# Optimization experiments

Measured on AMD Instinct MI355X. Metric: run time of the kernel, lower is better.

The kernel has to match this reference:

```python
import jax, jax.numpy as jnp
import numpy as np


def setup_inputs() -> dict:
    key = jax.random.key(0)
    k1, k2 = jax.random.split(key)
    # (t, h, w) per image/video; h, w divisible by spatial_merge_size=2
    grid_thw = jnp.asarray(np.array([[1, 64, 64], [4, 48, 48], [8, 32, 64], [16, 32, 32]], dtype=np.int64))
    num_grid_per_side = 35
    hidden = 1152
    pos_embed_weight = jax.random.normal(k1, (num_grid_per_side * num_grid_per_side, hidden), dtype=jnp.float32)
    quarter_head_dim = 32  # mrope_section [24,20,20] sums to 64 = 2*quarter_head_dim
    inv_freq = 1.0 / (10000.0 ** (jnp.arange(quarter_head_dim, dtype=jnp.float32) / quarter_head_dim))
    return {
        'grid_thw': grid_thw,
        'pos_embed_weight': pos_embed_weight,
        'inv_freq': inv_freq,
        'spatial_merge_size': 2,
        'num_grid_per_side': num_grid_per_side,
    }


def _forward(grid_np, pos_embed_weight, inv_freq, m, G):
    # grid_np: host numpy int array [num_images, 3] -> static per-image shapes
    D = pos_embed_weight.shape[-1]
    pieces = []
    coords_list = []
    for t, h, w in grid_np.tolist():
        # ---- 4-corner bilinear interpolation of pos embeddings ----
        h_idxs = jnp.linspace(0.0, G - 1, h)
        w_idxs = jnp.linspace(0.0, G - 1, w)
        hf = h_idxs.astype(jnp.int32)
        wf = w_idxs.astype(jnp.int32)
        hc = jnp.minimum(hf + 1, G - 1)
        wc = jnp.minimum(wf + 1, G - 1)
        dh = h_idxs - hf.astype(h_idxs.dtype)
        dw = w_idxs - wf.astype(w_idxs.dtype)
        idx = jnp.stack([
            (hf[:, None] * G + wf[None, :]).reshape(-1),
            (hf[:, None] * G + wc[None, :]).reshape(-1),
            (hc[:, None] * G + wf[None, :]).reshape(-1),
            (hc[:, None] * G + wc[None, :]).reshape(-1),
        ], 0)  # [4, h*w]
        wts = jnp.stack([
            ((1 - dh)[:, None] * (1 - dw)[None, :]).reshape(-1),
            ((1 - dh)[:, None] * dw[None, :]).reshape(-1),
            (dh[:, None] * (1 - dw)[None, :]).reshape(-1),
            (dh[:, None] * dw[None, :]).reshape(-1),
        ], 0).astype(pos_embed_weight.dtype)  # [4, h*w]
        pe = (pos_embed_weight[idx] * wts[:, :, None]).sum(0)  # [h*w, D]
        # ---- spatial-merge reshuffle, repeated over t frames ----
        pe = jnp.tile(pe, (t, 1)).reshape(t, h // m, m, w // m, m, D)
        pe = pe.transpose(0, 1, 3, 2, 4, 5).reshape(-1, D)
        pieces.append(pe)
        # ---- (row, col) position ids in merged-block order ----
        br = jnp.arange(h // m)
        bc = jnp.arange(w // m)
        im = jnp.arange(m)
        row = br[:, None, None, None] * m + im[None, None, :, None]
        col = bc[None, :, None, None] * m + im[None, None, None, :]
        row = jnp.broadcast_to(row, (h // m, w // m, m, m)).reshape(-1)
        col = jnp.broadcast_to(col, (h // m, w // m, m, m)).reshape(-1)
        coords = jnp.stack([row, col], -1)  # [h*w, 2]
        coords = jnp.tile(coords, (t, 1))   # [t*h*w, 2]
        coords_list.append(coords)
    patch_pos_embeds = jnp.concatenate(pieces, 0)   # [total_tokens, D]
    pos_ids = jnp.concatenate(coords_list, 0)       # [total_tokens, 2]
    max_hw = int(grid_np[:, 1:].max())
    seq = jnp.arange(max_hw, dtype=jnp.float32)
    freqs = seq[:, None] * inv_freq[None, :]        # [max_hw, Q]
    embeddings = freqs[pos_ids].reshape(pos_ids.shape[0], -1)  # [T, 2Q]
    # MRoPE section interleave: freqs_3d[0..2] are identical copies of
    # `embeddings`, so replacing strided slices of freqs_t with slices of the
    # other copies is a mathematical no-op: freqs_t == embeddings.
    emb = jnp.concatenate([embeddings, embeddings], -1)  # [T, head_dim]
    return patch_pos_embeds, jnp.cos(emb), jnp.sin(emb)


def reference(grid_thw, pos_embed_weight, inv_freq, spatial_merge_size, num_grid_per_side):
    grid_np = np.asarray(grid_thw)  # int grid sizes are static metadata
    return _forward(grid_np, pos_embed_weight, inv_freq, int(spatial_merge_size), int(num_grid_per_side))
```

## Files before the change

kernel.cpp:

```cpp
#include <hip/hip_runtime.h>


typedef float fx4 __attribute__((ext_vector_type(4)));

__device__ __forceinline__ void nt_store4(float* p, fx4 v) {
    __builtin_nontemporal_store(v, (fx4*)p);
}

template <int T, int H, int W, int OFF>
__device__ __forceinline__ void patch_body(int b, const float* __restrict__ tab,
                                           float* __restrict__ out) {
    constexpr int C4 = 1152 / 4;
    constexpr int HW = H * W;
    constexpr int WB = W / 2;

    int idx = b * 256 + (int)threadIdx.x;
    int tok = idx / C4;
    int c4  = idx - tok * C4;

    int j  = tok & 1;
    int i  = (tok >> 1) & 1;
    int blk = tok >> 2;
    int bw = blk % WB;
    int bh = blk / WB;
    int row = (bh << 1) + i;
    int col = (bw << 1) + j;

    float hx = (float)row * (float)(34.0 / (H - 1));
    float wx = (float)col * (float)(34.0 / (W - 1));
    int hf = (int)hx, wf = (int)wx;
    float dh = hx - (float)hf, dw = wx - (float)wf;
    int hc = min(hf + 1, 34), wc = min(wf + 1, 34);

    float w00 = (1.f - dh) * (1.f - dw);
    float w01 = (1.f - dh) * dw;
    float w10 = dh * (1.f - dw);
    float w11 = dh * dw;

    const fx4 a = *((const fx4*)(tab + (hf * 35 + wf) * 1152) + c4);
    const fx4 bq= *((const fx4*)(tab + (hf * 35 + wc) * 1152) + c4);
    const fx4 c = *((const fx4*)(tab + (hc * 35 + wf) * 1152) + c4);
    const fx4 d = *((const fx4*)(tab + (hc * 35 + wc) * 1152) + c4);

    fx4 o = w00 * a + w01 * bq + w10 * c + w11 * d;

    float* dst = out + (size_t)(OFF + tok) * 1152 + (c4 << 2);
    #pragma unroll
    for (int f = 0; f < T; ++f)
        nt_store4(dst + (size_t)f * (HW * 1152), o);
}

template <int T, int H, int W, int OFF>
__device__ __forceinline__ void rope_body(int b, const float* __restrict__ invf,
                                          float* __restrict__ cosO,
                                          float* __restrict__ sinO) {
    constexpr int HW = H * W;
    constexpr int WB = W / 2;

    int idx = b * 256 + (int)threadIdx.x;
    int tok = idx >> 4;
    int l4  = idx & 15;
    int rem = tok % HW;

    int j  = rem & 1;
    int i  = (rem >> 1) & 1;
    int blk = rem >> 2;
    int bw = blk % WB;
    int bh = blk / WB;
    int row = (bh << 1) + i;
    int col = (bw << 1) + j;

    float fp = (float)((l4 < 8) ? row : col);
    fx4 iv = ((const fx4*)invf)[l4 & 7];

    float s0, c0, s1, c1, s2, c2, s3, c3;
    __sincosf(fp * iv.x, &s0, &c0);
    __sincosf(fp * iv.y, &s1, &c1);
    __sincosf(fp * iv.z, &s2, &c2);
    __sincosf(fp * iv.w, &s3, &c3);
    fx4 cv = {c0, c1, c2, c3};
    fx4 sv = {s0, s1, s2, s3};

    size_t base = (size_t)(OFF + tok) * 128 + (l4 << 2);
    nt_store4(cosO + base,      cv);
    nt_store4(cosO + base + 64, cv);
    nt_store4(sinO + base,      sv);
    nt_store4(sinO + base + 64, sv);
}

__global__ __launch_bounds__(256) void fused_kernel(
    const float* __restrict__ tab, const float* __restrict__ invf,
    float* __restrict__ out, float* __restrict__ cosO, float* __restrict__ sinO)
{
    int b = (int)blockIdx.x;
    if      (b < 1152)  patch_body<16,32, 32, 29696>(b,         tab, out);
    else if (b < 3456)  patch_body<8, 32, 64, 13312>(b - 1152,  tab, out);
    else if (b < 6048)  patch_body<4, 48, 48, 4096> (b - 3456,  tab, out);
    else if (b < 7072)  rope_body<16,32, 32, 29696> (b - 6048,  invf, cosO, sinO);
    else if (b < 8096)  rope_body<8, 32, 64, 13312> (b - 7072,  invf, cosO, sinO);
    else if (b < 8672)  rope_body<4, 48, 48, 4096>  (b - 8096,  invf, cosO, sinO);
    else if (b < 8928)  rope_body<1, 64, 64, 0>     (b - 8672,  invf, cosO, sinO);
    else                patch_body<1, 64, 64, 0>    (b - 8928,  tab, out);
}

extern "C" void kernel_launch(void* const* d_in, const int* in_sizes, int n_in,
                              void* d_out, int out_size, void* d_ws, size_t ws_size,
                              hipStream_t stream) {
    const float* tab  = (const float*)d_in[1];
    const float* invf = (const float*)d_in[2];
    float* out = (float*)d_out;

    constexpr size_t NTOK = 46080;
    float* cosO = out + NTOK * 1152;
    float* sinO = cosO + NTOK * 128;

    fused_kernel<<<13536, 256, 0, stream>>>(tab, invf, out, cosO, sinO);
}
```

Baseline: 55.96 us.

## Share bilinear corner loads across 2x2 merge-block tokens in pos-embed interpolation

For images whose side is larger than the grid (step < 1), each thread now computes two or four adjacent tokens of a 2x2 merge block. It loads a 3x3 or 2x3 neighbourhood of table rows and reuses them through separable interpolation, where before every token loaded its own four corners. This cuts gather loads per output and roughly halves the block count. In exchange each thread does more work and holds more registers.

```diff
diff --git a/kernel.cpp b/kernel.cpp
--- a/kernel.cpp
+++ b/kernel.cpp
@@ -8,15 +8,132 @@
 }
 
 template <int T, int H, int W, int OFF>
-__device__ __forceinline__ void patch_body(int b, const float* __restrict__ tab,
-                                           float* __restrict__ out) {
-    constexpr int C4 = 1152 / 4;
-    constexpr int HW = H * W;
-    constexpr int WB = W / 2;
-
-    int idx = b * 256 + (int)threadIdx.x;
-    int tok = idx / C4;
-    int c4  = idx - tok * C4;
+__device__ __forceinline__ void pe_quad_body(int b, const float* __restrict__ tab,
+                                             float* __restrict__ out) {
+    static_assert(H > 35 && W > 35, "2x2 sharing needs step < 1 in both axes");
+    constexpr int HW = H * W;
+    constexpr int WB = W / 2;
+
+    int idx = b * 256 + (int)threadIdx.x;
+    int mb  = idx / 288;
+    int c4  = idx - mb * 288;
+    int bw  = mb % WB;
+    int bh  = mb / WB;
+
+    int row0 = bh << 1, col0 = bw << 1;
+
+    float hx0 = (float)row0 * (float)(34.0 / (H - 1));
+    float hx1 = (float)(row0 + 1) * (float)(34.0 / (H - 1));
+    float wx0 = (float)col0 * (float)(34.0 / (W - 1));
+    float wx1 = (float)(col0 + 1) * (float)(34.0 / (W - 1));
+
+    int hf0 = (int)hx0;  float dh0 = hx0 - (float)hf0;
+    int hf1 = (int)hx1;  float dh1 = hx1 - (float)hf1;
+    int oi  = hf1 - hf0;
+    int wf0 = (int)wx0;  float dw0 = wx0 - (float)wf0;
+    int wf1 = (int)wx1;  float dw1 = wx1 - (float)wf1;
+    int oj  = wf1 - wf0;
+
+    int r1 = min(hf0 + 1, 34), r2 = min(hf0 + 2, 34);
+    int c1 = min(wf0 + 1, 34), c2 = min(wf0 + 2, 34);
+
+    const float* base = tab + c4 * 4;
+    #define LD(r, c) (*((const fx4*)(base + (size_t)((r) * 35 + (c)) * 1152)))
+    fx4 P00 = LD(hf0, wf0), P01 = LD(hf0, c1), P02 = LD(hf0, c2);
+    fx4 P10 = LD(r1,  wf0), P11 = LD(r1,  c1), P12 = LD(r1,  c2);
+    fx4 P20 = LD(r2,  wf0), P21 = LD(r2,  c1), P22 = LD(r2,  c2);
+    #undef LD
+
+    float omdw0 = 1.f - dw0, omdw1 = 1.f - dw1;
+    fx4 a0 = omdw0 * P00 + dw0 * P01;
+    fx4 a1 = omdw0 * P10 + dw0 * P11;
+    fx4 a2 = omdw0 * P20 + dw0 * P21;
+    fx4 b0 = omdw1 * (oj ? P01 : P00) + dw1 * (oj ? P02 : P01);
+    fx4 b1 = omdw1 * (oj ? P11 : P10) + dw1 * (oj ? P12 : P11);
+    fx4 b2 = omdw1 * (oj ? P21 : P20) + dw1 * (oj ? P22 : P21);
+
+    float omdh0 = 1.f - dh0, omdh1 = 1.f - dh1;
+    fx4 o00 = omdh0 * a0 + dh0 * a1;
+    fx4 o01 = omdh0 * b0 + dh0 * b1;
+    fx4 ta = oi ? a1 : a0, ba = oi ? a2 : a1;
+    fx4 tb = oi ? b1 : b0, bb = oi ? b2 : b1;
+    fx4 o10 = omdh1 * ta + dh1 * ba;
+    fx4 o11 = omdh1 * tb + dh1 * bb;
+
+    float* d = out + (size_t)(OFF + (mb << 2)) * 1152 + (c4 << 2);
+    #pragma unroll
+    for (int f = 0; f < T; ++f) {
+        float* df = d + (size_t)f * (HW * 1152);
+        nt_store4(df,            o00);
+        nt_store4(df + 1152,     o01);
+        nt_store4(df + 2 * 1152, o10);
+        nt_store4(df + 3 * 1152, o11);
+    }
+}
+
+template <int T, int H, int W, int OFF>
+__device__ __forceinline__ void pe_cpair_body(int b, const float* __restrict__ tab,
+                                              float* __restrict__ out) {
+    static_assert(W > 35, "column sharing needs step < 1");
+    constexpr int HW = H * W;
+    constexpr int WB = W / 2;
+
+    int idx = b * 256 + (int)threadIdx.x;
+    int u   = idx / 288;
+    int c4  = idx - u * 288;
+    int i   = u & 1;
+    int mb  = u >> 1;
+    int bw  = mb % WB;
+    int bh  = mb / WB;
+
+    int row  = (bh << 1) + i;
+    int col0 = bw << 1;
+
+    float hx  = (float)row * (float)(34.0 / (H - 1));
+    float wx0 = (float)col0 * (float)(34.0 / (W - 1));
+    float wx1 = (float)(col0 + 1) * (float)(34.0 / (W - 1));
+
+    int hf = (int)hx;   float dh = hx - (float)hf;
+    int hc = min(hf + 1, 34);
+    int wf0 = (int)wx0; float dw0 = wx0 - (float)wf0;
+    int wf1 = (int)wx1; float dw1 = wx1 - (float)wf1;
+    int oj  = wf1 - wf0;
+    int c1 = min(wf0 + 1, 34), c2 = min(wf0 + 2, 34);
+
+    const float* base = tab + c4 * 4;
+    #define LD(r, c) (*((const fx4*)(base + (size_t)((r) * 35 + (c)) * 1152)))
+    fx4 Pf0 = LD(hf, wf0), Pf1 = LD(hf, c1), Pf2 = LD(hf, c2);
+    fx4 Pc0 = LD(hc, wf0), Pc1 = LD(hc, c1), Pc2 = LD(hc, c2);
+    #undef LD
+
+    float omdw0 = 1.f - dw0, omdw1 = 1.f - dw1, omdh = 1.f - dh;
+    fx4 qf = omdw0 * Pf0 + dw0 * Pf1;
+    fx4 qc = omdw0 * Pc0 + dw0 * Pc1;
+    fx4 sf = omdw1 * (oj ? Pf1 : Pf0) + dw1 * (oj ? Pf2 : Pf1);
+    fx4 sc = omdw1 * (oj ? Pc1 : Pc0) + dw1 * (oj ? Pc2 : Pc1);
+
+    fx4 o0 = omdh * qf + dh * qc;
+    fx4 o1 = omdh * sf + dh * sc;
+
+    int tok0 = OFF + (mb << 2) + (i << 1);
+    float* d = out + (size_t)tok0 * 1152 + (c4 << 2);
+    #pragma unroll
+    for (int f = 0; f < T; ++f) {
+        float* df = d + (size_t)f * (HW * 1152);
+        nt_store4(df,        o0);
+        nt_store4(df + 1152, o1);
+    }
+}
+
+template <int T, int H, int W, int OFF>
+__device__ __forceinline__ void pe_body(int b, const float* __restrict__ tab,
+                                        float* __restrict__ out) {
+    constexpr int HW = H * W;
+    constexpr int WB = W / 2;
+
+    int idx = b * 256 + (int)threadIdx.x;
+    int tok = idx / 288;
+    int c4  = idx - tok * 288;
 
     int j  = tok & 1;
     int i  = (tok >> 1) & 1;
@@ -37,10 +154,10 @@
     float w10 = dh * (1.f - dw);
     float w11 = dh * dw;
 
-    const fx4 a = *((const fx4*)(tab + (hf * 35 + wf) * 1152) + c4);
-    const fx4 bq= *((const fx4*)(tab + (hf * 35 + wc) * 1152) + c4);
-    const fx4 c = *((const fx4*)(tab + (hc * 35 + wf) * 1152) + c4);
-    const fx4 d = *((const fx4*)(tab + (hc * 35 + wc) * 1152) + c4);
+    const fx4 a = *((const fx4*)(tab + (size_t)(hf * 35 + wf) * 1152) + c4);
+    const fx4 bq= *((const fx4*)(tab + (size_t)(hf * 35 + wc) * 1152) + c4);
+    const fx4 c = *((const fx4*)(tab + (size_t)(hc * 35 + wf) * 1152) + c4);
+    const fx4 d = *((const fx4*)(tab + (size_t)(hc * 35 + wc) * 1152) + c4);
 
     fx4 o = w00 * a + w01 * bq + w10 * c + w11 * d;
 
@@ -93,14 +210,14 @@
     float* __restrict__ out, float* __restrict__ cosO, float* __restrict__ sinO)
 {
     int b = (int)blockIdx.x;
-    if      (b < 1152)  patch_body<16,32, 32, 29696>(b,         tab, out);
-    else if (b < 3456)  patch_body<8, 32, 64, 13312>(b - 1152,  tab, out);
-    else if (b < 6048)  patch_body<4, 48, 48, 4096> (b - 3456,  tab, out);
-    else if (b < 7072)  rope_body<16,32, 32, 29696> (b - 6048,  invf, cosO, sinO);
-    else if (b < 8096)  rope_body<8, 32, 64, 13312> (b - 7072,  invf, cosO, sinO);
-    else if (b < 8672)  rope_body<4, 48, 48, 4096>  (b - 8096,  invf, cosO, sinO);
-    else if (b < 8928)  rope_body<1, 64, 64, 0>     (b - 8672,  invf, cosO, sinO);
-    else                patch_body<1, 64, 64, 0>    (b - 8928,  tab, out);
+    if      (b < 1152)  pe_body<16,32, 32, 29696>      (b,         tab, out);
+    else if (b < 2304)  pe_cpair_body<8, 32, 64, 13312>(b - 1152,  tab, out);
+    else if (b < 2952)  pe_quad_body<4, 48, 48, 4096>  (b - 2304,  tab, out);
+    else if (b < 3976)  rope_body<16,32, 32, 29696>    (b - 2952,  invf, cosO, sinO);
+    else if (b < 5000)  rope_body<8, 32, 64, 13312>    (b - 3976,  invf, cosO, sinO);
+    else if (b < 5576)  rope_body<4, 48, 48, 4096>     (b - 5000,  invf, cosO, sinO);
+    else if (b < 5832)  rope_body<1, 64, 64, 0>        (b - 5576,  invf, cosO, sinO);
+    else                pe_quad_body<1, 64, 64, 0>     (b - 5832,  tab, out);
 }
 
 extern "C" void kernel_launch(void* const* d_in, const int* in_sizes, int n_in,
@@ -114,5 +231,5 @@
     float* cosO = out + NTOK * 1152;
     float* sinO = cosO + NTOK * 128;
 
-    fused_kernel<<<13536, 256, 0, stream>>>(tab, invf, out, cosO, sinO);
-}
+    fused_kernel<<<6984, 256, 0, stream>>>(tab, invf, out, cosO, sinO);
+}
```

New measurement: 53.24 us. 4.8% less time.
